# Kernel tuning notes

Measured on AMD Instinct MI355X. Metric: run time of the kernel, lower is better.

The kernel has to match this reference:

```python
import jax, jax.numpy as jnp
import numpy as np

B, S, D, H, FF = 4, 1024, 1024, 16, 4096
DH = D // H
EPS = 1e-5


def setup_inputs() -> dict:
    key = jax.random.key(0)
    ks = jax.random.split(key, 24)
    w = lambda i, shp: jax.random.normal(ks[i], shp, jnp.float32) * 0.02
    inp = {
        'tgt': jax.random.normal(ks[0], (B, S, D), jnp.float32),
        'memory': jax.random.normal(ks[1], (B, S, D), jnp.float32),
        'mask': jax.random.randint(ks[2], (B, S, S), 0, 2, jnp.int32),
        # self-attention projections (stored [in,out]; torch Linear weight transposed)
        'sa_wq': w(3, (D, D)), 'sa_bq': jnp.zeros((D,), jnp.float32),
        'sa_wk': w(4, (D, D)), 'sa_bk': jnp.zeros((D,), jnp.float32),
        'sa_wv': w(5, (D, D)), 'sa_bv': jnp.zeros((D,), jnp.float32),
        'sa_wo': w(6, (D, D)), 'sa_bo': jnp.zeros((D,), jnp.float32),
        # cross-attention projections
        'ca_wq': w(7, (D, D)), 'ca_bq': jnp.zeros((D,), jnp.float32),
        'ca_wk': w(8, (D, D)), 'ca_bk': jnp.zeros((D,), jnp.float32),
        'ca_wv': w(9, (D, D)), 'ca_bv': jnp.zeros((D,), jnp.float32),
        'ca_wo': w(10, (D, D)), 'ca_bo': jnp.zeros((D,), jnp.float32),
        # FFN
        'w1': w(11, (D, FF)), 'b1': jnp.zeros((FF,), jnp.float32),
        'w2': w(12, (FF, D)), 'b2': jnp.zeros((D,), jnp.float32),
        # LayerNorms
        'g1': jnp.ones((D,), jnp.float32), 'be1': jnp.zeros((D,), jnp.float32),
        'g2': jnp.ones((D,), jnp.float32), 'be2': jnp.zeros((D,), jnp.float32),
        'g3': jnp.ones((D,), jnp.float32), 'be3': jnp.zeros((D,), jnp.float32),
    }
    return inp


def _layernorm(x, g, b):
    m = jnp.mean(x, axis=-1, keepdims=True)
    v = jnp.mean((x - m) ** 2, axis=-1, keepdims=True)
    return (x - m) * jax.lax.rsqrt(v + EPS) * g + b


def _mha(x, y, mask, wq, bq, wk, bk, wv, bv, wo, bo):
    # chunk(h,-1)+cat(0) head-split == reshape to [B,S,H,DH]
    b_, sq, _ = x.shape
    sk = y.shape[1]
    q = (x @ wq + bq).reshape(b_, sq, H, DH)
    k = (y @ wk + bk).reshape(b_, sk, H, DH)
    v = (y @ wv + bv).reshape(b_, sk, H, DH)
    score = jnp.einsum('bqhd,bkhd->bhqk', q, k) / jnp.float32(np.sqrt(DH))
    score = score + (1.0 - mask[:, None].astype(score.dtype)) * (-1e9)
    attn = jax.nn.softmax(score, axis=-1)
    out = jnp.einsum('bhqk,bkhd->bqhd', attn, v).reshape(b_, sq, D)
    return out @ wo + bo


def reference(tgt, memory, mask,
              sa_wq, sa_bq, sa_wk, sa_bk, sa_wv, sa_bv, sa_wo, sa_bo,
              ca_wq, ca_bq, ca_wk, ca_bk, ca_wv, ca_bv, ca_wo, ca_bo,
              w1, b1, w2, b2, g1, be1, g2, be2, g3, be3):
    t = tgt + _mha(tgt, tgt, mask, sa_wq, sa_bq, sa_wk, sa_bk, sa_wv, sa_bv, sa_wo, sa_bo)
    t = _layernorm(t, g1, be1)
    t = t + _mha(t, memory, mask, ca_wq, ca_bq, ca_wk, ca_bk, ca_wv, ca_bv, ca_wo, ca_bo)
    t = _layernorm(t, g2, be2)
    t = t + (jax.nn.relu(t @ w1 + b1) @ w2 + b2)
    t = _layernorm(t, g3, be3)
    return t
```

## Files before the change

kernel.cpp:

```cpp
#include <hip/hip_runtime.h>
#include <math.h>

typedef float f32x4 __attribute__((ext_vector_type(4)));
typedef unsigned short ushort8 __attribute__((ext_vector_type(8)));
typedef unsigned short ushort4v __attribute__((ext_vector_type(4)));
typedef __bf16 bf16x8 __attribute__((ext_vector_type(8)));
typedef unsigned int u32;

__device__ __forceinline__ unsigned short f2bf(float x) {
  union { float f; unsigned u; } v; v.f = x;
  unsigned r = v.u + 0x7FFFu + ((v.u >> 16) & 1u);
  return (unsigned short)(r >> 16);
}
__device__ __forceinline__ float bf2f(unsigned short u) {
  union { unsigned u; float f; } c; c.u = ((unsigned)u) << 16; return c.f;
}

__device__ __forceinline__ f32x4 mfma16(ushort8 a, ushort8 b, f32x4 c) {
  return __builtin_amdgcn_mfma_f32_16x16x32_bf16(
      __builtin_bit_cast(bf16x8, a), __builtin_bit_cast(bf16x8, b), c, 0, 0, 0);
}

__device__ __forceinline__ void gload16(const void* g, void* l) {
  __builtin_amdgcn_global_load_lds((const __attribute__((address_space(1))) u32*)g,
                                   (__attribute__((address_space(3))) u32*)l, 16, 0, 0);
}

__global__ __launch_bounds__(256) void gemm_bf16_kernel(
    const unsigned short* __restrict__ A, const unsigned short* __restrict__ Bt,
    const float* __restrict__ bias, void* __restrict__ C,
    int M, int N, int K, int flags)
{
  __shared__ __align__(16) char As0[128 * 128];
  __shared__ __align__(16) char Bs0[128 * 128];
  __shared__ __align__(16) char As1[128 * 128];
  __shared__ __align__(16) char Bs1[128 * 128];
  const int bn = blockIdx.x, bm = blockIdx.y;
  const int t = threadIdx.x;
  const int lane = t & 63, w = t >> 6, wm = w >> 1, wn = w & 1;
  const int l4 = lane & 15, lg = lane >> 4;
  const size_t K2 = (size_t)K * 2;

  f32x4 acc[4][4];
#pragma unroll
  for (int i = 0; i < 4; ++i)
#pragma unroll
    for (int j = 0; j < 4; ++j) acc[i][j] = f32x4{0.f, 0.f, 0.f, 0.f};

  const int lr = lane >> 3;
  const int ls = (lane & 7) ^ lr;
  const char* Ag = (const char*)A + (size_t)(bm * 128 + w * 32 + lr) * K2 + ls * 16;
  const char* Bg = (const char*)Bt + (size_t)(bn * 128 + w * 32 + lr) * K2 + ls * 16;
  const int wo = w * 4096;

  auto STAGE = [&](char* Al, char* Bl, int kt) {
    const size_t ko = (size_t)kt * 128;
#pragma unroll
    for (int i = 0; i < 4; ++i) {
      gload16(Ag + i * 8 * K2 + ko, Al + wo + i * 1024);
      gload16(Bg + i * 8 * K2 + ko, Bl + wo + i * 1024);
    }
  };
  auto COMPUTE = [&](const char* As, const char* Bs) {
#pragma unroll
    for (int ks = 0; ks < 2; ++ks) {
      const int kb = ks * 64 + lg * 16;
      ushort8 af[4], bfr[4];
#pragma unroll
      for (int mi = 0; mi < 4; ++mi) {
        int r = wm * 64 + mi * 16 + l4;
        af[mi] = *reinterpret_cast<const ushort8*>(As + r * 128 + (kb ^ ((r & 7) << 4)));
      }
#pragma unroll
      for (int ni = 0; ni < 4; ++ni) {
        int r = wn * 64 + ni * 16 + l4;
        bfr[ni] = *reinterpret_cast<const ushort8*>(Bs + r * 128 + (kb ^ ((r & 7) << 4)));
      }
#pragma unroll
      for (int mi = 0; mi < 4; ++mi)
#pragma unroll
        for (int ni = 0; ni < 4; ++ni)
          acc[mi][ni] = mfma16(af[mi], bfr[ni], acc[mi][ni]);
    }
  };

  const int nkt = K >> 6;
  STAGE(As0, Bs0, 0);
  __syncthreads();
  for (int kt = 0; kt < nkt; kt += 2) {
    STAGE(As1, Bs1, kt + 1);
    COMPUTE(As0, Bs0);
    __syncthreads();
    if (kt + 2 < nkt) STAGE(As0, Bs0, kt + 2);
    COMPUTE(As1, Bs1);
    __syncthreads();
  }

  const int relu = flags & 1, obf = flags & 2;
#pragma unroll
  for (int mi = 0; mi < 4; ++mi)
#pragma unroll
    for (int ni = 0; ni < 4; ++ni) {
      int col = bn * 128 + wn * 64 + ni * 16 + l4;
      float bia = bias[col];
#pragma unroll
      for (int j = 0; j < 4; ++j) {
        int row = bm * 128 + wm * 64 + mi * 16 + lg * 4 + j;
        float vv = acc[mi][ni][j] + bia;
        if (relu) vv = fmaxf(vv, 0.f);
        if (obf) ((unsigned short*)C)[(size_t)row * N + col] = f2bf(vv);
        else     ((float*)C)[(size_t)row * N + col] = vv;
      }
    }
}

constexpr int kS = 1024, kD = 1024, kDH = 64;

__global__ __launch_bounds__(256) void attn_kernel(
    const unsigned short* __restrict__ Qg, const unsigned short* __restrict__ Kg,
    const unsigned short* __restrict__ Vg, int qs, int ks_,
    const unsigned short* __restrict__ mbias, unsigned short* __restrict__ Og)
{
  __shared__ __align__(16) char Qs[8192];
  __shared__ __align__(16) char Ks0[8192];
  __shared__ __align__(16) char Ks1[8192];
  __shared__ __align__(16) char Ms0[8192];
  __shared__ __align__(16) char Ms1[8192];
  __shared__ __align__(16) char VT0[8192];
  __shared__ __align__(16) char VT1[8192];
  __shared__ __align__(16) char Ps[8192];
  const int qt = blockIdx.x, h = blockIdx.y, b = blockIdx.z;
  const int t = threadIdx.x, lane = t & 63, w = t >> 6;
  const int l4 = lane & 15, lg = lane >> 4;
  const int lr = lane >> 3, sg = (lane & 7) ^ lr;

  {
    int r = t >> 2, c0 = (t & 3) * 16;
    const unsigned short* src = Qg + (size_t)(b * kS + qt * 64 + r) * qs + h * kDH + c0;
#pragma unroll
    for (int hf = 0; hf < 2; ++hf) {
      ushort8 v = *reinterpret_cast<const ushort8*>(src + hf * 8);
      int c = c0 + hf * 8;
      *reinterpret_cast<ushort8*>(Qs + r * 128 + ((c * 2) ^ ((r & 7) << 4))) = v;
    }
  }

  auto stageK = [&](char* Kl, int kt) {
    const char* base = (const char*)(Kg + (size_t)(b * kS + kt * 64) * ks_ + h * kDH) + sg * 16;
    gload16(base + (size_t)(w * 16 + lr) * (ks_ * 2), Kl + w * 2048);
    gload16(base + (size_t)(w * 16 + 8 + lr) * (ks_ * 2), Kl + w * 2048 + 1024);
  };
  auto stageM = [&](char* Ml, int kt) {
    const char* base = (const char*)mbias + ((size_t)(b * 1024 + qt * 64) * 1024 + kt * 64) * 2
                       + (lane & 7) * 16;
    gload16(base + (size_t)(w * 16 + lr) * 2048, Ml + w * 2048);
    gload16(base + (size_t)(w * 16 + 8 + lr) * 2048, Ml + w * 2048 + 1024);
  };

  float m_r[4], l_r[4];
  f32x4 o[4];
#pragma unroll
  for (int j = 0; j < 4; ++j) { m_r[j] = -1e30f; l_r[j] = 0.f; }
#pragma unroll
  for (int di = 0; di < 4; ++di) o[di] = f32x4{0.f, 0.f, 0.f, 0.f};

  ushort8 vA0, vA1, vB0, vB1;
  stageK(Ks0, 0);
  stageM(Ms0, 0);
  {
    const unsigned short* vsrc = Vg + (size_t)(b * kS + (t >> 2)) * ks_ + h * kDH + (t & 3) * 16;
    vA0 = *reinterpret_cast<const ushort8*>(vsrc);
    vA1 = *reinterpret_cast<const ushort8*>(vsrc + 8);
  }

#define ATTN_TILE(KC, MC, VC, KN, MN, VC0, VC1, VN0, VN1, KTV)                           \
  {                                                                                      \
    asm volatile("s_waitcnt vmcnt(0)" ::: "memory");                                     \
    __builtin_amdgcn_s_barrier();                                                        \
    __builtin_amdgcn_sched_barrier(0);                                                   \
    {                                      \
      int key2 = (t >> 2) * 2, c0 = (t & 3) * 16;                                        \
      _Pragma("unroll")                                                                  \
      for (int i = 0; i < 8; ++i) {                                                      \
        int dh = c0 + i;                                                                 \
        *(unsigned short*)(VC + dh * 128 +                                               \
            (key2 ^ ((dh & 7) << 4) ^ ((dh >> 4) << 5))) = VC0[i];                       \
      }                                                                                  \
      _Pragma("unroll")                                                                  \
      for (int i = 0; i < 8; ++i) {                                                      \
        int dh = c0 + 8 + i;                                                             \
        *(unsigned short*)(VC + dh * 128 +                                               \
            (key2 ^ ((dh & 7) << 4) ^ ((dh >> 4) << 5))) = VC1[i];                       \
      }                                                                                  \
    }                                                                                    \
    if ((KTV) + 1 < 16) {                  \
      stageK(KN, (KTV) + 1);                                                             \
      stageM(MN, (KTV) + 1);                                                             \
      const unsigned short* vsrc = Vg +                                                  \
          (size_t)(b * kS + ((KTV) + 1) * 64 + (t >> 2)) * ks_ + h * kDH + (t & 3) * 16; \
      VN0 = *reinterpret_cast<const ushort8*>(vsrc);                                     \
      VN1 = *reinterpret_cast<const ushort8*>(vsrc + 8);                                 \
    }                                                                                    \
    f32x4 sc[4];                                                                         \
    _Pragma("unroll")                                                                    \
    for (int ni = 0; ni < 4; ++ni) sc[ni] = f32x4{0.f, 0.f, 0.f, 0.f};                   \
    __builtin_amdgcn_s_setprio(1);                                                       \
    _Pragma("unroll")                                                                    \
    for (int ks = 0; ks < 2; ++ks) {                                                     \
      const int kb = ks * 64 + lg * 16;                                                  \
      int qr = w * 16 + l4;                                                              \
      ushort8 a = *(const ushort8*)(Qs + qr * 128 + (kb ^ ((qr & 7) << 4)));             \
      _Pragma("unroll")                                                                  \
      for (int ni = 0; ni < 4; ++ni) {                                                   \
        int kr = ni * 16 + l4;                                                           \
        ushort8 bb = *(const ushort8*)(KC + kr * 128 + (kb ^ ((kr & 7) << 4)));          \
        sc[ni] = mfma16(a, bb, sc[ni]);                                                  \
      }                                                                                  \
    }                                                                                    \
    __builtin_amdgcn_s_setprio(0);                                                       \
    float pmax[4];                                                                       \
    _Pragma("unroll")                                                                    \
    for (int j = 0; j < 4; ++j) {                                                        \
      int row = lg * 4 + j;                                                              \
      _Pragma("unroll")                                                                  \
      for (int ni = 0; ni < 4; ++ni) {                                                   \
        int col = ni * 16 + l4;                                                          \
        unsigned short mu = *(const unsigned short*)(MC + w * 2048 + row * 128 +         \
            ((col * 2) ^ ((row & 7) << 4) ^ ((row & 8) << 2)));                          \
        sc[ni][j] += bf2f(mu);                                                           \
      }                                                                                  \
      pmax[j] = fmaxf(fmaxf(sc[0][j], sc[1][j]), fmaxf(sc[2][j], sc[3][j]));             \
    }                                                                                    \
    _Pragma("unroll")                                                                    \
    for (int j = 0; j < 4; ++j) {                                                        \
      pmax[j] = fmaxf(pmax[j], __shfl_xor(pmax[j], 1, 64));                              \
      pmax[j] = fmaxf(pmax[j], __shfl_xor(pmax[j], 2, 64));                              \
      pmax[j] = fmaxf(pmax[j], __shfl_xor(pmax[j], 4, 64));                              \
      pmax[j] = fmaxf(pmax[j], __shfl_xor(pmax[j], 8, 64));                              \
    }                                                                                    \
    bool need = (pmax[0] > m_r[0] + 8.f) || (pmax[1] > m_r[1] + 8.f) ||                  \
                (pmax[2] > m_r[2] + 8.f) || (pmax[3] > m_r[3] + 8.f);                    \
    if (__any(need)) {                                                                   \
      _Pragma("unroll")                                                                  \
      for (int j = 0; j < 4; ++j) {                                                      \
        float mn = fmaxf(m_r[j], pmax[j]);                                               \
        float al = exp2f(m_r[j] - mn);                                                   \
        m_r[j] = mn; l_r[j] *= al;                                                       \
        o[0][j] *= al; o[1][j] *= al; o[2][j] *= al; o[3][j] *= al;                      \
      }                                                                                  \
    }                                                                                    \
    float rsum[4] = {0.f, 0.f, 0.f, 0.f};                                                \
    _Pragma("unroll")                                                                    \
    for (int ni = 0; ni < 4; ++ni)                                                       \
      _Pragma("unroll")                                                                  \
      for (int j = 0; j < 4; ++j) {                                                      \
        float p = exp2f(sc[ni][j] - m_r[j]);                                             \
        sc[ni][j] = p;                                                                   \
        rsum[j] += p;                                                                    \
      }                                                                                  \
    _Pragma("unroll")                                                                    \
    for (int j = 0; j < 4; ++j) {                                                        \
      rsum[j] += __shfl_xor(rsum[j], 1, 64);                                             \
      rsum[j] += __shfl_xor(rsum[j], 2, 64);                                             \
      rsum[j] += __shfl_xor(rsum[j], 4, 64);                                             \
      rsum[j] += __shfl_xor(rsum[j], 8, 64);                                             \
      l_r[j] += rsum[j];                                                                 \
    }                                                                                    \
    {                               \
      char* Pw = Ps + w * 2048;                                                          \
      _Pragma("unroll")                                                                  \
      for (int ni = 0; ni < 4; ++ni)                                                     \
        _Pragma("unroll")                                                                \
        for (int j = 0; j < 4; ++j) {                                                    \
          int row = lg * 4 + j, col = ni * 16 + l4;                                      \
          *(unsigned short*)(Pw + row * 128 +                                            \
              ((col * 2) ^ ((row & 7) << 4) ^ ((row & 8) << 2))) =                       \
              __builtin_bit_cast(unsigned short, (__bf16)sc[ni][j]);                     \
        }                                                                                \
    }                                                                                    \
    asm volatile("s_waitcnt lgkmcnt(0)" ::: "memory");                                   \
    __builtin_amdgcn_s_barrier();                                                        \
    __builtin_amdgcn_sched_barrier(0);                                                   \
    __builtin_amdgcn_s_setprio(1);                                                       \
    {                                                                                    \
      const char* Pw = Ps + w * 2048;                                                    \
      _Pragma("unroll")                                                                  \
      for (int ks = 0; ks < 2; ++ks) {                                                   \
        const int kb = ks * 64 + lg * 16;                                                \
        ushort8 pa = *(const ushort8*)(Pw + l4 * 128 +                                   \
            (kb ^ ((l4 & 7) << 4) ^ ((l4 & 8) << 2)));                                   \
        _Pragma("unroll")                                                                \
        for (int di = 0; di < 4; ++di) {                                                 \
          int vr2 = di * 16 + l4;                                                        \
          ushort8 vb = *(const ushort8*)(VC + vr2 * 128 +                                \
              (kb ^ ((vr2 & 7) << 4) ^ ((vr2 >> 4) << 5)));                              \
          o[di] = mfma16(pa, vb, o[di]);                                                 \
        }                                                                                \
      }                                                                                  \
    }                                                                                    \
    __builtin_amdgcn_s_setprio(0);                                                       \
  }

  for (int kt = 0; kt < 16; kt += 2) {
    ATTN_TILE(Ks0, Ms0, VT0, Ks1, Ms1, vA0, vA1, vB0, vB1, kt);
    ATTN_TILE(Ks1, Ms1, VT1, Ks0, Ms0, vB0, vB1, vA0, vA1, kt + 1);
  }
#undef ATTN_TILE

  float rinv[4];
#pragma unroll
  for (int j = 0; j < 4; ++j) rinv[j] = 1.0f / l_r[j];
#pragma unroll
  for (int di = 0; di < 4; ++di) {
    int col = h * kDH + di * 16 + l4;
#pragma unroll
    for (int j = 0; j < 4; ++j) {
      int qrow = qt * 64 + w * 16 + lg * 4 + j;
      Og[(size_t)(b * kS + qrow) * kD + col] =
          __builtin_bit_cast(unsigned short, (__bf16)(o[di][j] * rinv[j]));
    }
  }
}

__global__ __launch_bounds__(256) void addln_kernel(
    const float* __restrict__ x, const unsigned short* __restrict__ y,
    const float* __restrict__ g, const float* __restrict__ be,
    float* __restrict__ out, unsigned short* __restrict__ ob)
{
  const int row = blockIdx.x, t = threadIdx.x;
  const size_t base = (size_t)row * 1024 + t * 4;
  float4 xv = *reinterpret_cast<const float4*>(x + base);
  ushort4v yv = *reinterpret_cast<const ushort4v*>(y + base);
  float v0 = xv.x + bf2f(yv[0]), v1 = xv.y + bf2f(yv[1]);
  float v2 = xv.z + bf2f(yv[2]), v3 = xv.w + bf2f(yv[3]);
  float s1 = v0 + v1 + v2 + v3;
  float s2 = v0 * v0 + v1 * v1 + v2 * v2 + v3 * v3;
#pragma unroll
  for (int off = 1; off < 64; off <<= 1) {
    s1 += __shfl_xor(s1, off, 64);
    s2 += __shfl_xor(s2, off, 64);
  }
  __shared__ float r1[4], r2[4];
  const int w = t >> 6, lane = t & 63;
  if (lane == 0) { r1[w] = s1; r2[w] = s2; }
  __syncthreads();
  s1 = r1[0] + r1[1] + r1[2] + r1[3];
  s2 = r2[0] + r2[1] + r2[2] + r2[3];
  const float mean = s1 * (1.0f / 1024.0f);
  const float var = s2 * (1.0f / 1024.0f) - mean * mean;
  const float rs = rsqrtf(var + 1e-5f);
  float4 gv = *reinterpret_cast<const float4*>(g + t * 4);
  float4 bv = *reinterpret_cast<const float4*>(be + t * 4);
  float4 ov;
  ov.x = (v0 - mean) * rs * gv.x + bv.x;
  ov.y = (v1 - mean) * rs * gv.y + bv.y;
  ov.z = (v2 - mean) * rs * gv.z + bv.z;
  ov.w = (v3 - mean) * rs * gv.w + bv.w;
  *reinterpret_cast<float4*>(out + base) = ov;
  if (ob) {
    ushort4v bo;
    bo[0] = f2bf(ov.x); bo[1] = f2bf(ov.y); bo[2] = f2bf(ov.z); bo[3] = f2bf(ov.w);
    *reinterpret_cast<ushort4v*>(ob + base) = bo;
  }
}

__global__ __launch_bounds__(256) void cvt2_bf16_kernel(
    const float* __restrict__ a, const float* __restrict__ b,
    unsigned short* __restrict__ da, unsigned short* __restrict__ db, int n8each)
{
  int i = blockIdx.x * 256 + threadIdx.x;
  const float* s = a; unsigned short* d = da;
  if (i >= n8each) { s = b; d = db; i -= n8each; }
  if (i >= n8each) return;
  float4 f0 = reinterpret_cast<const float4*>(s)[i * 2];
  float4 f1 = reinterpret_cast<const float4*>(s)[i * 2 + 1];
  ushort8 v;
  v[0] = f2bf(f0.x); v[1] = f2bf(f0.y); v[2] = f2bf(f0.z); v[3] = f2bf(f0.w);
  v[4] = f2bf(f1.x); v[5] = f2bf(f1.y); v[6] = f2bf(f1.z); v[7] = f2bf(f1.w);
  reinterpret_cast<ushort8*>(d)[i] = v;
}

__global__ __launch_bounds__(256) void transpose_cvt_kernel(
    const float* __restrict__ src, unsigned short* __restrict__ dst, int K, int N)
{
  __shared__ float tile[32][33];
  const int bx = blockIdx.x, by = blockIdx.y;
  const int tx = threadIdx.x & 31, ty = threadIdx.x >> 5;
#pragma unroll
  for (int i = 0; i < 4; ++i)
    tile[ty + i * 8][tx] = src[(size_t)(by * 32 + ty + i * 8) * N + bx * 32 + tx];
  __syncthreads();
#pragma unroll
  for (int i = 0; i < 4; ++i)
    dst[(size_t)(bx * 32 + ty + i * 8) * K + by * 32 + tx] = f2bf(tile[tx][ty + i * 8]);
}

struct TPtrs { const float* s[8]; unsigned short* d[8]; float scale[8]; };
__global__ __launch_bounds__(256) void tcvt_batch_kernel(TPtrs p)
{
  __shared__ float tile[32][33];
  const float* __restrict__ src = p.s[blockIdx.z];
  unsigned short* __restrict__ dst = p.d[blockIdx.z];
  const float sc = p.scale[blockIdx.z];
  const int bx = blockIdx.x, by = blockIdx.y;
  const int tx = threadIdx.x & 31, ty = threadIdx.x >> 5;
#pragma unroll
  for (int i = 0; i < 4; ++i)
    tile[ty + i * 8][tx] = src[(size_t)(by * 32 + ty + i * 8) * 1024 + bx * 32 + tx];
  __syncthreads();
#pragma unroll
  for (int i = 0; i < 4; ++i)
    dst[(size_t)(bx * 32 + ty + i * 8) * 1024 + by * 32 + tx] = f2bf(tile[tx][ty + i * 8] * sc);
}

__global__ void biasprep_kernel(const float* sq, const float* sk, const float* sv,
                                const float* cq, const float* ck, const float* cv,
                                float* bsa, float* bca, float* bcq, float s)
{
  int i = blockIdx.x * 256 + threadIdx.x;
  if (i < 1024) { bsa[i] = sq[i] * s; bcq[i] = cq[i] * s; bca[i] = ck[i]; bca[i + 1024] = cv[i]; }
  else if (i < 2048) bsa[i] = sk[i - 1024];
  else if (i < 3072) bsa[i] = sv[i - 2048];
}

__global__ __launch_bounds__(256) void maskprep_kernel(
    const int* __restrict__ mask, unsigned short* __restrict__ mbias)
{
  int idx = blockIdx.x * 256 + threadIdx.x;
  int chunk = idx & 127;
  int q = (idx >> 7) & 1023;
  int b = idx >> 17;
  int tile = chunk >> 3, slot = chunk & 7;
  int sslot = slot ^ (q & 7) ^ ((q & 8) >> 2);
  const int* src = mask + ((size_t)(b * 1024 + q) * 1024) + tile * 64 + sslot * 8;
  int4 m0 = *reinterpret_cast<const int4*>(src);
  int4 m1 = *reinterpret_cast<const int4*>(src + 4);
  const unsigned short NEG = 0xCE6E;
  ushort8 v;
  v[0] = m0.x ? 0 : NEG; v[1] = m0.y ? 0 : NEG; v[2] = m0.z ? 0 : NEG; v[3] = m0.w ? 0 : NEG;
  v[4] = m1.x ? 0 : NEG; v[5] = m1.y ? 0 : NEG; v[6] = m1.z ? 0 : NEG; v[7] = m1.w ? 0 : NEG;
  *reinterpret_cast<ushort8*>(mbias + (size_t)idx * 8) = v;
}

extern "C" void kernel_launch(void* const* d_in, const int* in_sizes, int n_in,
                              void* d_out, int out_size, void* d_ws, size_t ws_size,
                              hipStream_t stream)
{
  const float* tgt  = (const float*)d_in[0];
  const float* memi = (const float*)d_in[1];
  const int*   mask = (const int*)d_in[2];
  const float* sa_wq = (const float*)d_in[3];  const float* sa_bq = (const float*)d_in[4];
  const float* sa_wk = (const float*)d_in[5];  const float* sa_bk = (const float*)d_in[6];
  const float* sa_wv = (const float*)d_in[7];  const float* sa_bv = (const float*)d_in[8];
  const float* sa_wo = (const float*)d_in[9];  const float* sa_bo = (const float*)d_in[10];
  const float* ca_wq = (const float*)d_in[11]; const float* ca_bq = (const float*)d_in[12];
  const float* ca_wk = (const float*)d_in[13]; const float* ca_bk = (const float*)d_in[14];
  const float* ca_wv = (const float*)d_in[15]; const float* ca_bv = (const float*)d_in[16];
  const float* ca_wo = (const float*)d_in[17]; const float* ca_bo = (const float*)d_in[18];
  const float* w1 = (const float*)d_in[19]; const float* b1 = (const float*)d_in[20];
  const float* w2 = (const float*)d_in[21]; const float* b2 = (const float*)d_in[22];
  const float* g1 = (const float*)d_in[23]; const float* be1 = (const float*)d_in[24];
  const float* g2 = (const float*)d_in[25]; const float* be2 = (const float*)d_in[26];
  const float* g3 = (const float*)d_in[27]; const float* be3 = (const float*)d_in[28];
  float* out = (float*)d_out;
  char* W = (char*)d_ws;
  const size_t MB = 1 << 20;
  typedef unsigned short us;
  const float QSCALE = 0.18033688011112042f;

  us* Wsaqkv = (us*)(W + 0);
  us* Wsao   = (us*)(W + 6 * MB);
  us* Wcaq   = (us*)(W + 8 * MB);
  us* Wcakv  = (us*)(W + 10 * MB);
  us* Wcao   = (us*)(W + 14 * MB);
  us* W1t    = (us*)(W + 16 * MB);
  us* W2t    = (us*)(W + 24 * MB);
  float* b_saqkv = (float*)(W + 32 * MB);
  float* b_cakv  = (float*)(W + 32 * MB + 16384);
  float* b_caq   = (float*)(W + 32 * MB + 32768);
  us* tgt_bf = (us*)(W + 33 * MB);
  us* T2b    = tgt_bf;
  us* mem_bf = (us*)(W + 41 * MB);
  us* QKV    = (us*)(W + 49 * MB);
  us* Qca    = (us*)(W + 49 * MB);
  us* KVca   = (us*)(W + 57 * MB);
  us* T1b    = (us*)(W + 65 * MB);
  us* AO     = (us*)(W + 73 * MB);
  us* Hb     = (us*)(W + 49 * MB);
  us* Opb    = (us*)(W + 81 * MB);
  us* mbias  = (us*)(W + 89 * MB);
  float* T1f = (float*)(W + 98 * MB);
  float* T2f = T1f;

  const int M = 4096;
  dim3 blk(256);
  auto gemm = [&](const us* Aa, const us* Bta, const float* bias, void* Cc,
                  int Nn, int Kk, int flags) {
    gemm_bf16_kernel<<<dim3(Nn / 128, M / 128), blk, 0, stream>>>(Aa, Bta, bias, Cc, M, Nn, Kk, flags);
  };

  TPtrs tp;
  tp.s[0] = sa_wq; tp.d[0] = Wsaqkv;              tp.scale[0] = QSCALE;
  tp.s[1] = sa_wk; tp.d[1] = Wsaqkv + 1024 * 1024; tp.scale[1] = 1.f;
  tp.s[2] = sa_wv; tp.d[2] = Wsaqkv + 2048 * 1024; tp.scale[2] = 1.f;
  tp.s[3] = sa_wo; tp.d[3] = Wsao;                 tp.scale[3] = 1.f;
  tp.s[4] = ca_wq; tp.d[4] = Wcaq;                 tp.scale[4] = QSCALE;
  tp.s[5] = ca_wk; tp.d[5] = Wcakv;                tp.scale[5] = 1.f;
  tp.s[6] = ca_wv; tp.d[6] = Wcakv + 1024 * 1024;  tp.scale[6] = 1.f;
  tp.s[7] = ca_wo; tp.d[7] = Wcao;                 tp.scale[7] = 1.f;
  tcvt_batch_kernel<<<dim3(32, 32, 8), blk, 0, stream>>>(tp);
  transpose_cvt_kernel<<<dim3(128, 32), blk, 0, stream>>>(w1, W1t, 1024, 4096);
  transpose_cvt_kernel<<<dim3(32, 128), blk, 0, stream>>>(w2, W2t, 4096, 1024);
  cvt2_bf16_kernel<<<dim3(4096), blk, 0, stream>>>(tgt, memi, tgt_bf, mem_bf, M * 1024 / 8);
  biasprep_kernel<<<dim3(12), blk, 0, stream>>>(sa_bq, sa_bk, sa_bv, ca_bq, ca_bk, ca_bv,
                                                b_saqkv, b_cakv, b_caq, QSCALE);
  maskprep_kernel<<<dim3(2048), blk, 0, stream>>>(mask, mbias);

  gemm(tgt_bf, Wsaqkv, b_saqkv, QKV, 3072, 1024, 2);
  attn_kernel<<<dim3(16, 16, 4), blk, 0, stream>>>(QKV, QKV + 1024, QKV + 2048, 3072, 3072, mbias, AO);
  gemm(AO, Wsao, sa_bo, Opb, 1024, 1024, 2);
  addln_kernel<<<dim3(M), blk, 0, stream>>>(tgt, Opb, g1, be1, T1f, T1b);

  gemm(T1b, Wcaq, b_caq, Qca, 1024, 1024, 2);
  gemm(mem_bf, Wcakv, b_cakv, KVca, 2048, 1024, 2);
  attn_kernel<<<dim3(16, 16, 4), blk, 0, stream>>>(Qca, KVca, KVca + 1024, 1024, 2048, mbias, AO);
  gemm(AO, Wcao, ca_bo, Opb, 1024, 1024, 2);
  addln_kernel<<<dim3(M), blk, 0, stream>>>(T1f, Opb, g2, be2, T2f, T2b);

  gemm(T2b, W1t, b1, Hb, 4096, 1024, 3);
  gemm(Hb, W2t, b2, Opb, 1024, 4096, 2);
  addln_kernel<<<dim3(M), blk, 0, stream>>>(T2f, Opb, g3, be3, out, nullptr);

  (void)in_sizes; (void)n_in; (void)out_size; (void)ws_size;
}
```

Baseline: 464.9 us.

## Pack mask bias in MFMA fragment order and keep Q in registers

```diff
diff --git a/kernel.cpp b/kernel.cpp
--- a/kernel.cpp
+++ b/kernel.cpp
@@ -116,16 +116,13 @@
 
 constexpr int kS = 1024, kD = 1024, kDH = 64;
 
-__global__ __launch_bounds__(256) void attn_kernel(
+__global__ __launch_bounds__(256, 4) void attn_kernel(
     const unsigned short* __restrict__ Qg, const unsigned short* __restrict__ Kg,
     const unsigned short* __restrict__ Vg, int qs, int ks_,
-    const unsigned short* __restrict__ mbias, unsigned short* __restrict__ Og)
-{
-  __shared__ __align__(16) char Qs[8192];
+    const unsigned short* __restrict__ mpack, unsigned short* __restrict__ Og)
+{
   __shared__ __align__(16) char Ks0[8192];
   __shared__ __align__(16) char Ks1[8192];
-  __shared__ __align__(16) char Ms0[8192];
-  __shared__ __align__(16) char Ms1[8192];
   __shared__ __align__(16) char VT0[8192];
   __shared__ __align__(16) char VT1[8192];
   __shared__ __align__(16) char Ps[8192];
@@ -134,28 +131,19 @@
   const int l4 = lane & 15, lg = lane >> 4;
   const int lr = lane >> 3, sg = (lane & 7) ^ lr;
 
+  ushort8 q0, q1;
   {
-    int r = t >> 2, c0 = (t & 3) * 16;
-    const unsigned short* src = Qg + (size_t)(b * kS + qt * 64 + r) * qs + h * kDH + c0;
-#pragma unroll
-    for (int hf = 0; hf < 2; ++hf) {
-      ushort8 v = *reinterpret_cast<const ushort8*>(src + hf * 8);
-      int c = c0 + hf * 8;
-      *reinterpret_cast<ushort8*>(Qs + r * 128 + ((c * 2) ^ ((r & 7) << 4))) = v;
-    }
-  }
+    const unsigned short* src = Qg + (size_t)(b * kS + qt * 64 + w * 16 + l4) * qs + h * kDH;
+    q0 = *reinterpret_cast<const ushort8*>(src + lg * 8);
+    q1 = *reinterpret_cast<const ushort8*>(src + 32 + lg * 8);
+  }
+  const unsigned short* mtile = mpack + (size_t)(b * 16 + qt) * 65536 + t * 16;
 
   auto stageK = [&](char* Kl, int kt) {
     const char* base = (const char*)(Kg + (size_t)(b * kS + kt * 64) * ks_ + h * kDH) + sg * 16;
     gload16(base + (size_t)(w * 16 + lr) * (ks_ * 2), Kl + w * 2048);
     gload16(base + (size_t)(w * 16 + 8 + lr) * (ks_ * 2), Kl + w * 2048 + 1024);
   };
-  auto stageM = [&](char* Ml, int kt) {
-    const char* base = (const char*)mbias + ((size_t)(b * 1024 + qt * 64) * 1024 + kt * 64) * 2
-                       + (lane & 7) * 16;
-    gload16(base + (size_t)(w * 16 + lr) * 2048, Ml + w * 2048);
-    gload16(base + (size_t)(w * 16 + 8 + lr) * 2048, Ml + w * 2048 + 1024);
-  };
 
   float m_r[4], l_r[4];
   f32x4 o[4];
@@ -164,16 +152,17 @@
 #pragma unroll
   for (int di = 0; di < 4; ++di) o[di] = f32x4{0.f, 0.f, 0.f, 0.f};
 
-  ushort8 vA0, vA1, vB0, vB1;
+  ushort8 vA0, vA1, vB0, vB1, mA0, mA1, mB0, mB1;
   stageK(Ks0, 0);
-  stageM(Ms0, 0);
   {
     const unsigned short* vsrc = Vg + (size_t)(b * kS + (t >> 2)) * ks_ + h * kDH + (t & 3) * 16;
     vA0 = *reinterpret_cast<const ushort8*>(vsrc);
     vA1 = *reinterpret_cast<const ushort8*>(vsrc + 8);
-  }
-
-#define ATTN_TILE(KC, MC, VC, KN, MN, VC0, VC1, VN0, VN1, KTV)                           \
+    mA0 = *reinterpret_cast<const ushort8*>(mtile);
+    mA1 = *reinterpret_cast<const ushort8*>(mtile + 8);
+  }
+
+#define ATTN_TILE(KC, VC, KN, VC0, VC1, VN0, VN1, MC0, MC1, MN0, MN1, KTV)               \
   {                                                                                      \
     asm volatile("s_waitcnt vmcnt(0)" ::: "memory");                                     \
     __builtin_amdgcn_s_barrier();                                                        \
@@ -195,11 +184,12 @@
     }                                                                                    \
     if ((KTV) + 1 < 16) {                  \
       stageK(KN, (KTV) + 1);                                                             \
-      stageM(MN, (KTV) + 1);                                                             \
       const unsigned short* vsrc = Vg +                                                  \
           (size_t)(b * kS + ((KTV) + 1) * 64 + (t >> 2)) * ks_ + h * kDH + (t & 3) * 16; \
       VN0 = *reinterpret_cast<const ushort8*>(vsrc);                                     \
       VN1 = *reinterpret_cast<const ushort8*>(vsrc + 8);                                 \
+      MN0 = *reinterpret_cast<const ushort8*>(mtile + ((KTV) + 1) * 4096);               \
+      MN1 = *reinterpret_cast<const ushort8*>(mtile + ((KTV) + 1) * 4096 + 8);           \
     }                                                                                    \
     f32x4 sc[4];                                                                         \
     _Pragma("unroll")                                                                    \
@@ -208,8 +198,7 @@
     _Pragma("unroll")                                                                    \
     for (int ks = 0; ks < 2; ++ks) {                                                     \
       const int kb = ks * 64 + lg * 16;                                                  \
-      int qr = w * 16 + l4;                                                              \
-      ushort8 a = *(const ushort8*)(Qs + qr * 128 + (kb ^ ((qr & 7) << 4)));             \
+      ushort8 a = ks ? q1 : q0;                                                          \
       _Pragma("unroll")                                                                  \
       for (int ni = 0; ni < 4; ++ni) {                                                   \
         int kr = ni * 16 + l4;                                                           \
@@ -221,14 +210,10 @@
     float pmax[4];                                                                       \
     _Pragma("unroll")                                                                    \
     for (int j = 0; j < 4; ++j) {                                                        \
-      int row = lg * 4 + j;                                                              \
-      _Pragma("unroll")                                                                  \
-      for (int ni = 0; ni < 4; ++ni) {                                                   \
-        int col = ni * 16 + l4;                                                          \
-        unsigned short mu = *(const unsigned short*)(MC + w * 2048 + row * 128 +         \
-            ((col * 2) ^ ((row & 7) << 4) ^ ((row & 8) << 2)));                          \
-        sc[ni][j] += bf2f(mu);                                                           \
-      }                                                                                  \
+      sc[0][j] += bf2f(MC0[j]);                                                          \
+      sc[1][j] += bf2f(MC0[4 + j]);                                                      \
+      sc[2][j] += bf2f(MC1[j]);                                                          \
+      sc[3][j] += bf2f(MC1[4 + j]);                                                      \
       pmax[j] = fmaxf(fmaxf(sc[0][j], sc[1][j]), fmaxf(sc[2][j], sc[3][j]));             \
     }                                                                                    \
     _Pragma("unroll")                                                                    \
@@ -302,8 +287,8 @@
   }
 
   for (int kt = 0; kt < 16; kt += 2) {
-    ATTN_TILE(Ks0, Ms0, VT0, Ks1, Ms1, vA0, vA1, vB0, vB1, kt);
-    ATTN_TILE(Ks1, Ms1, VT1, Ks0, Ms0, vB0, vB1, vA0, vA1, kt + 1);
+    ATTN_TILE(Ks0, VT0, Ks1, vA0, vA1, vB0, vB1, mA0, mA1, mB0, mB1, kt);
+    ATTN_TILE(Ks1, VT1, Ks0, vB0, vB1, vA0, vA1, mB0, mB1, mA0, mA1, kt + 1);
   }
 #undef ATTN_TILE
 
@@ -424,22 +409,29 @@
 }
 
 __global__ __launch_bounds__(256) void maskprep_kernel(
-    const int* __restrict__ mask, unsigned short* __restrict__ mbias)
+    const int* __restrict__ mask, unsigned short* __restrict__ mpack)
 {
   int idx = blockIdx.x * 256 + threadIdx.x;
-  int chunk = idx & 127;
-  int q = (idx >> 7) & 1023;
-  int b = idx >> 17;
-  int tile = chunk >> 3, slot = chunk & 7;
-  int sslot = slot ^ (q & 7) ^ ((q & 8) >> 2);
-  const int* src = mask + ((size_t)(b * 1024 + q) * 1024) + tile * 64 + sslot * 8;
-  int4 m0 = *reinterpret_cast<const int4*>(src);
-  int4 m1 = *reinterpret_cast<const int4*>(src + 4);
+  int t = idx & 255;
+  int kt = (idx >> 8) & 15;
+  int qt = (idx >> 12) & 15;
+  int b = idx >> 16;
+  int qb = qt * 64 + ((t >> 6) & 3) * 16 + ((t >> 4) & 3) * 4;
+  int kb = kt * 64 + (t & 15);
   const unsigned short NEG = 0xCE6E;
-  ushort8 v;
-  v[0] = m0.x ? 0 : NEG; v[1] = m0.y ? 0 : NEG; v[2] = m0.z ? 0 : NEG; v[3] = m0.w ? 0 : NEG;
-  v[4] = m1.x ? 0 : NEG; v[5] = m1.y ? 0 : NEG; v[6] = m1.z ? 0 : NEG; v[7] = m1.w ? 0 : NEG;
-  *reinterpret_cast<ushort8*>(mbias + (size_t)idx * 8) = v;
+  ushort8 v0, v1;
+#pragma unroll
+  for (int ni = 0; ni < 2; ++ni)
+#pragma unroll
+    for (int j = 0; j < 4; ++j)
+      v0[ni * 4 + j] = mask[(size_t)(b * 1024 + qb + j) * 1024 + kb + ni * 16] ? 0 : NEG;
+#pragma unroll
+  for (int ni = 2; ni < 4; ++ni)
+#pragma unroll
+    for (int j = 0; j < 4; ++j)
+      v1[(ni - 2) * 4 + j] = mask[(size_t)(b * 1024 + qb + j) * 1024 + kb + ni * 16] ? 0 : NEG;
+  reinterpret_cast<ushort8*>(mpack)[idx * 2] = v0;
+  reinterpret_cast<ushort8*>(mpack)[idx * 2 + 1] = v1;
 }
 
 extern "C" void kernel_launch(void* const* d_in, const int* in_sizes, int n_in,
@@ -488,7 +480,7 @@
   us* AO     = (us*)(W + 73 * MB);
   us* Hb     = (us*)(W + 49 * MB);
   us* Opb    = (us*)(W + 81 * MB);
-  us* mbias  = (us*)(W + 89 * MB);
+  us* mpack  = (us*)(W + 89 * MB);
   float* T1f = (float*)(W + 98 * MB);
   float* T2f = T1f;
 
@@ -514,16 +506,16 @@
   cvt2_bf16_kernel<<<dim3(4096), blk, 0, stream>>>(tgt, memi, tgt_bf, mem_bf, M * 1024 / 8);
   biasprep_kernel<<<dim3(12), blk, 0, stream>>>(sa_bq, sa_bk, sa_bv, ca_bq, ca_bk, ca_bv,
                                                 b_saqkv, b_cakv, b_caq, QSCALE);
-  maskprep_kernel<<<dim3(2048), blk, 0, stream>>>(mask, mbias);
+  maskprep_kernel<<<dim3(1024), blk, 0, stream>>>(mask, mpack);
 
   gemm(tgt_bf, Wsaqkv, b_saqkv, QKV, 3072, 1024, 2);
-  attn_kernel<<<dim3(16, 16, 4), blk, 0, stream>>>(QKV, QKV + 1024, QKV + 2048, 3072, 3072, mbias, AO);
+  attn_kernel<<<dim3(16, 16, 4), blk, 0, stream>>>(QKV, QKV + 1024, QKV + 2048, 3072, 3072, mpack, AO);
   gemm(AO, Wsao, sa_bo, Opb, 1024, 1024, 2);
   addln_kernel<<<dim3(M), blk, 0, stream>>>(tgt, Opb, g1, be1, T1f, T1b);
 
   gemm(T1b, Wcaq, b_caq, Qca, 1024, 1024, 2);
   gemm(mem_bf, Wcakv, b_cakv, KVca, 2048, 1024, 2);
-  attn_kernel<<<dim3(16, 16, 4), blk, 0, stream>>>(Qca, KVca, KVca + 1024, 1024, 2048, mbias, AO);
+  attn_kernel<<<dim3(16, 16, 4), blk, 0, stream>>>(Qca, KVca, KVca + 1024, 1024, 2048, mpack, AO);
   gemm(AO, Wcao, ca_bo, Opb, 1024, 1024, 2);
   addln_kernel<<<dim3(M), blk, 0, stream>>>(T1f, Opb, g2, be2, T2f, T2b);
 
```

New measurement: 538.7 us. 15.9% more time.
